# Performance work log

Measured on AMD Instinct MI355X. Metric: run time of the kernel, lower is better.

The kernel has to match this reference:

```python
import jax, jax.numpy as jnp
import numpy as np

HEADS = 16
HIDDEN = 1024
DH = HIDDEN // HEADS
EPS = 1e-6


def setup_inputs() -> dict:
    key = jax.random.key(0)
    ks = jax.random.split(key, 18)
    B, S, D, H = 8, 4096, HIDDEN, HEADS
    std = 0.02
    inp = {
        "x": jax.random.normal(ks[0], (B, S, D), dtype=jnp.float32),
        "mask": jnp.zeros((B, 1, S), dtype=jnp.float32),
        "Wq": std * jax.random.normal(ks[1], (D, D), dtype=jnp.float32),
        "bq": jnp.zeros((D,), jnp.float32),
        "Wk": std * jax.random.normal(ks[2], (D, D), dtype=jnp.float32),
        "bk": jnp.zeros((D,), jnp.float32),
        "Wv": std * jax.random.normal(ks[3], (D, D), dtype=jnp.float32),
        "bv": jnp.zeros((D,), jnp.float32),
        "Wa": std * jax.random.normal(ks[4], (D, H), dtype=jnp.float32),
        "ba": jnp.zeros((H,), jnp.float32),
        "Wb": std * jax.random.normal(ks[5], (D, H), dtype=jnp.float32),
        "bb": jnp.zeros((H,), jnp.float32),
        "Wu": std * jax.random.normal(ks[6], (D, D), dtype=jnp.float32),
        "bu": jnp.zeros((D,), jnp.float32),
        "Wo": std * jax.random.normal(ks[7], (D, D), dtype=jnp.float32),
        "bo": jnp.zeros((D,), jnp.float32),
        "ln_g": jnp.ones((D,), jnp.float32),
        "ln_b": jnp.zeros((D,), jnp.float32),
    }
    return inp


def reference(x, mask, Wq, bq, Wk, bk, Wv, bv, Wa, ba, Wb, bb, Wu, bu, Wo, bo, ln_g, ln_b):
    B, S, D = x.shape
    H, dh = HEADS, D // HEADS
    scale = (D / H) ** -0.5

    q = x @ Wq + bq  # [B,S,D]
    k = x @ Wk + bk
    v = x @ Wv + bv

    # alpha pooling of q
    ascore = jnp.swapaxes((q @ Wa + ba) * scale, 1, 2) + mask  # [B,H,S]
    aw = jax.nn.softmax(ascore, axis=-1)
    qh = q.reshape(B, S, H, dh)
    q_av = jnp.einsum("bhs,bshd->bhd", aw, qh).reshape(B, 1, D)  # global query

    p = k * q_av  # [B,S,D], broadcast over seq

    # beta pooling of p
    bscore = jnp.swapaxes((p @ Wb + bb) * scale, 1, 2) + mask  # [B,H,S]
    bw = jax.nn.softmax(bscore, axis=-1)
    ph = p.reshape(B, S, H, dh)
    p_av = jnp.einsum("bhs,bshd->bhd", bw, ph).reshape(B, 1, D)  # global key

    u = p_av * v  # [B,S,D]
    r = u @ Wu + bu
    attn_out = (r + q) @ Wo + bo

    y = x + attn_out  # residual (dropout is identity at inference)
    mu = jnp.mean(y, axis=-1, keepdims=True)
    var = jnp.mean(jnp.square(y - mu), axis=-1, keepdims=True)
    return (y - mu) * jax.lax.rsqrt(var + EPS) * ln_g + ln_b
```

## Files before the change

### kernel.cpp

```cpp
#include <hip/hip_runtime.h>

typedef unsigned short u16;
typedef __bf16 bf16x8 __attribute__((ext_vector_type(8)));
typedef float  f32x4  __attribute__((ext_vector_type(4)));

__device__ __forceinline__ float b2f(u16 u) {
    unsigned int v = ((unsigned int)u) << 16;
    return __builtin_bit_cast(float, v);
}
__device__ __forceinline__ u16 f2b(float f) {
    unsigned int v = __builtin_bit_cast(unsigned int, f);
    v += 0x7fffu + ((v >> 16) & 1u);
    return (u16)(v >> 16);
}

#define GLD16(gp, lp) __builtin_amdgcn_global_load_lds( \
    (const __attribute__((address_space(1))) void*)(gp), \
    (__attribute__((address_space(3))) void*)(lp), 16, 0, 0)


__global__ __launch_bounds__(256) void convert_x(const float* __restrict__ x,
                                                 u16* __restrict__ xb) {
    size_t i = ((size_t)blockIdx.x * 256 + threadIdx.x) * 8;
    float4 v0 = *(const float4*)(x + i);
    float4 v1 = *(const float4*)(x + i + 4);
    ushort4 o0, o1;
    o0.x = f2b(v0.x); o0.y = f2b(v0.y); o0.z = f2b(v0.z); o0.w = f2b(v0.w);
    o1.x = f2b(v1.x); o1.y = f2b(v1.y); o1.z = f2b(v1.z); o1.w = f2b(v1.w);
    *(ushort4*)(xb + i)     = o0;
    *(ushort4*)(xb + i + 4) = o1;
}

__global__ __launch_bounds__(256) void transpose_w(const float* __restrict__ W,
                                                   u16* __restrict__ Wt) {
    __shared__ float tile[64][65];
    int kt = (blockIdx.x & 15) * 64;
    int nt = (blockIdx.x >> 4) * 64;
    int tid = threadIdx.x;
    int r = tid >> 4, c4 = (tid & 15) * 4;
    #pragma unroll
    for (int p = 0; p < 4; ++p) {
        int k = kt + p * 16 + r;
        float4 v = *(const float4*)(W + (size_t)k * 1024 + nt + c4);
        tile[c4 + 0][p * 16 + r] = v.x;
        tile[c4 + 1][p * 16 + r] = v.y;
        tile[c4 + 2][p * 16 + r] = v.z;
        tile[c4 + 3][p * 16 + r] = v.w;
    }
    __syncthreads();
    #pragma unroll
    for (int p = 0; p < 4; ++p) {
        int nl = p * 16 + r;
        ushort4 o;
        o.x = f2b(tile[nl][c4 + 0]); o.y = f2b(tile[nl][c4 + 1]);
        o.z = f2b(tile[nl][c4 + 2]); o.w = f2b(tile[nl][c4 + 3]);
        *(ushort4*)(Wt + (size_t)(nt + nl) * 1024 + kt + c4) = o;
    }
}

__global__ __launch_bounds__(256) void wu_prime(const float* __restrict__ Wu,
                                                const float* __restrict__ p_av,
                                                u16* __restrict__ Wut) {
    __shared__ float tile[64][65];
    int kt = (blockIdx.x & 15) * 64;
    int nt = (blockIdx.x >> 4) * 64;
    int tid = threadIdx.x;
    int r = tid >> 4, c4 = (tid & 15) * 4;
    #pragma unroll
    for (int p = 0; p < 4; ++p) {
        int k = kt + p * 16 + r;
        float4 v = *(const float4*)(Wu + (size_t)k * 1024 + nt + c4);
        tile[c4 + 0][p * 16 + r] = v.x;
        tile[c4 + 1][p * 16 + r] = v.y;
        tile[c4 + 2][p * 16 + r] = v.z;
        tile[c4 + 3][p * 16 + r] = v.w;
    }
    __syncthreads();
    for (int b = 0; b < 8; ++b) {
        float4 pv = *(const float4*)(p_av + (size_t)b * 1024 + kt + c4);
        #pragma unroll
        for (int p = 0; p < 4; ++p) {
            int nl = p * 16 + r;
            ushort4 o;
            o.x = f2b(tile[nl][c4 + 0] * pv.x);
            o.y = f2b(tile[nl][c4 + 1] * pv.y);
            o.z = f2b(tile[nl][c4 + 2] * pv.z);
            o.w = f2b(tile[nl][c4 + 3] * pv.w);
            *(ushort4*)(Wut + ((size_t)b * 1024 + nt + nl) * 1024 + kt + c4) = o;
        }
    }
}

__global__ __launch_bounds__(256) void wat_prep(const float* __restrict__ Wa,
                                                u16* __restrict__ Wat) {
    int idx = blockIdx.x * 256 + threadIdx.x;
    int h = idx >> 10, k = idx & 1023;
    Wat[idx] = f2b(Wa[(k << 4) + h]);
}

__global__ __launch_bounds__(256) void wbt_prep(const float* __restrict__ Wb,
                                                const float* __restrict__ q_av,
                                                u16* __restrict__ Wbt) {
    int idx = blockIdx.x * 256 + threadIdx.x;
    int b = idx >> 14, rem = idx & 16383;
    int h = rem >> 10, k = rem & 1023;
    Wbt[idx] = f2b(Wb[(k << 4) + h] * q_av[(b << 10) + k]);
}

__global__ __launch_bounds__(256) void bias_concat(const float* __restrict__ bq,
                                                   const float* __restrict__ bk,
                                                   const float* __restrict__ bv,
                                                   float* __restrict__ outb) {
    int i = blockIdx.x * 256 + threadIdx.x;
    outb[i] = (i < 1024) ? bq[i] : (i < 2048 ? bk[i - 1024] : bv[i - 2048]);
}

__global__ __launch_bounds__(256, 4)
void gemm_bf16(const u16* __restrict__ A, int lda,
               const u16* __restrict__ Bt,
               const float* __restrict__ bias,
               const u16* __restrict__ addsrc, int ldadd,
               u16* __restrict__ C, int ldc,
               int N, int K, int batch_rows) {
    __shared__ u16 As[128 * 64];
    __shared__ u16 Bs[128 * 64];
    int ntiles = N >> 7;
    int bid = blockIdx.x;
    int mtiles = gridDim.x / ntiles;
    int tm, tn;
    if ((mtiles & 7) == 0) {
        int xcd = bid & 7, s = bid >> 3;
        int mper = mtiles >> 3;
        tm = xcd * mper + s / ntiles;
        tn = s - (s / ntiles) * ntiles;
    } else {
        tm = bid / ntiles; tn = bid - (bid / ntiles) * ntiles;
    }
    int m0 = tm << 7, n0 = tn << 7;
    if (batch_rows > 0) Bt += (size_t)(m0 / batch_rows) * (size_t)N * K;
    int tid = threadIdx.x, lane = tid & 63, w = tid >> 6;
    int wm = (w >> 1) << 6, wn = (w & 1) << 6;
    int quad = lane >> 4, l16 = lane & 15;
    int rph = l16 & 7;
    int lrow = lane >> 3;
    int lkg  = (lane & 7) ^ lrow;

    int idxA = (m0 + (w << 5) + lrow) * lda + (lkg << 3);
    int idxB = (n0 + (w << 5) + lrow) * K   + (lkg << 3);
    int stepA = lda << 3, stepB = K << 3;

    f32x4 zero = {0.f, 0.f, 0.f, 0.f};
    f32x4 acc[4][4];
    #pragma unroll
    for (int i = 0; i < 4; ++i)
        #pragma unroll
        for (int j = 0; j < 4; ++j) acc[i][j] = zero;

    for (int kt = 0; kt < K; kt += 64) {
        __syncthreads();
        #pragma unroll
        for (int j = 0; j < 4; ++j) {
            int c = (w << 2) + j;
            GLD16(A  + (idxA + j * stepA + kt), &As[c << 9]);
            GLD16(Bt + (idxB + j * stepB + kt), &Bs[c << 9]);
        }
        __syncthreads();
        #pragma unroll
        for (int kk = 0; kk < 2; ++kk) {
            bf16x8 a[4], b[4];
            int kg = (((kk << 2) + quad) ^ rph) << 3;
            #pragma unroll
            for (int i = 0; i < 4; ++i) {
                a[i] = *(const bf16x8*)&As[((wm + (i << 4) + l16) << 6) + kg];
                b[i] = *(const bf16x8*)&Bs[((wn + (i << 4) + l16) << 6) + kg];
            }
            #pragma unroll
            for (int mi = 0; mi < 4; ++mi)
                #pragma unroll
                for (int ni = 0; ni < 4; ++ni)
                    acc[mi][ni] = __builtin_amdgcn_mfma_f32_16x16x32_bf16(
                        a[mi], b[ni], acc[mi][ni], 0, 0, 0);
        }
    }
    #pragma unroll
    for (int mi = 0; mi < 4; ++mi) {
        #pragma unroll
        for (int ni = 0; ni < 4; ++ni) {
            int col = n0 + wn + (ni << 4) + l16;
            float bv = bias[col];
            #pragma unroll
            for (int rg = 0; rg < 4; ++rg) {
                int rowg = m0 + wm + (mi << 4) + (quad << 2) + rg;
                float vv = acc[mi][ni][rg] + bv;
                if (addsrc) vv += b2f(addsrc[(size_t)rowg * ldadd + col]);
                C[(size_t)rowg * ldc + col] = f2b(vv);
            }
        }
    }
}

__global__ __launch_bounds__(256)
void score_gemm(const u16* __restrict__ A, int lda,
                const u16* __restrict__ Bt,
                const float* __restrict__ bias16,
                const float* __restrict__ mask,
                float* __restrict__ outsc,
                int batched) {
    __shared__ u16 As[64 * 64];
    __shared__ u16 Bs[16 * 64];
    int m0 = blockIdx.x << 6;
    int tid = threadIdx.x, lane = tid & 63, w = tid >> 6;
    int quad = lane >> 4, l16 = lane & 15;
    int rph = l16 & 7;
    int lrow = lane >> 3;
    int lkg  = (lane & 7) ^ lrow;
    const u16* Bb = Bt + (batched ? ((size_t)(m0 >> 12) << 14) : 0);

    int idxA = (m0 + (w << 4) + lrow) * lda + (lkg << 3);
    int stepA = lda << 3;
    int idxB = lrow * 1024 + (lkg << 3);

    f32x4 acc4 = (f32x4){0.f, 0.f, 0.f, 0.f};

    for (int kt = 0; kt < 1024; kt += 64) {
        __syncthreads();
        #pragma unroll
        for (int j = 0; j < 2; ++j) {
            int c = (w << 1) + j;
            GLD16(A + (idxA + j * stepA + kt), &As[c << 9]);
        }
        if (w < 2)
            GLD16(Bb + (idxB + w * 8192 + kt), &Bs[w << 9]);
        __syncthreads();
        #pragma unroll
        for (int kk = 0; kk < 2; ++kk) {
            int kg = (((kk << 2) + quad) ^ rph) << 3;
            bf16x8 b = *(const bf16x8*)&Bs[(l16 << 6) + kg];
            bf16x8 a = *(const bf16x8*)&As[(((w << 4) + l16) << 6) + kg];
            acc4 = __builtin_amdgcn_mfma_f32_16x16x32_bf16(a, b, acc4, 0, 0, 0);
        }
    }
    int bidx = m0 >> 12;
    float bv = bias16[l16];
    float* orow = outsc + (((size_t)bidx << 4) + l16) * 4096;
    const float* mrow = mask + ((size_t)bidx << 12);
    int sbase = (m0 & 4095) + (w << 4) + (quad << 2);
    #pragma unroll
    for (int rg = 0; rg < 4; ++rg)
        orow[sbase + rg] = 0.125f * (acc4[rg] + bv) + mrow[sbase + rg];
}

__global__ __launch_bounds__(256)
void softmax_kernel(float* __restrict__ score) {
    __shared__ float wbuf[4096];
    __shared__ float red[4];
    int tid = threadIdx.x, lane = tid & 63, w = tid >> 6;
    float* srow = score + (size_t)blockIdx.x * 4096;
    float mx = -1e30f;
    for (int s = tid; s < 4096; s += 256) mx = fmaxf(mx, srow[s]);
    for (int o = 32; o; o >>= 1) mx = fmaxf(mx, __shfl_xor(mx, o));
    if (lane == 0) red[w] = mx;
    __syncthreads();
    mx = fmaxf(fmaxf(red[0], red[1]), fmaxf(red[2], red[3]));
    __syncthreads();
    float sm = 0.f;
    for (int s = tid; s < 4096; s += 256) {
        float e = __expf(srow[s] - mx);
        wbuf[s] = e;
        sm += e;
    }
    for (int o = 32; o; o >>= 1) sm += __shfl_xor(sm, o);
    if (lane == 0) red[w] = sm;
    __syncthreads();
    float inv = 1.f / (red[0] + red[1] + red[2] + red[3]);
    for (int s = tid; s < 4096; s += 256) srow[s] = wbuf[s] * inv;
}

__global__ __launch_bounds__(256)
void pool_sum(const float* __restrict__ wn,
              const u16* __restrict__ X, int ldx,
              float* __restrict__ part) {
    __shared__ float psum[16][64];
    int blk = blockIdx.x, tid = threadIdx.x;
    int cc = blk & 7, bh = blk >> 3;
    int b = bh >> 4, h = bh & 15;
    const float* wrow = wn + ((size_t)bh << 12) + (cc << 9);
    int dg = (tid & 15) << 2;
    int sc = tid >> 4;
    const u16* base = X + (size_t)((b << 12) + (cc << 9) + (sc << 5)) * ldx + (h << 6) + dg;
    float a0 = 0, a1 = 0, a2 = 0, a3 = 0;
    for (int s = 0; s < 32; ++s) {
        float wv = wrow[(sc << 5) + s];
        ushort4 uv = *(const ushort4*)(base + (size_t)s * ldx);
        a0 += wv * b2f(uv.x); a1 += wv * b2f(uv.y);
        a2 += wv * b2f(uv.z); a3 += wv * b2f(uv.w);
    }
    psum[sc][dg + 0] = a0; psum[sc][dg + 1] = a1;
    psum[sc][dg + 2] = a2; psum[sc][dg + 3] = a3;
    __syncthreads();
    if (tid < 64) {
        float t = 0.f;
        #pragma unroll
        for (int j = 0; j < 16; ++j) t += psum[j][tid];
        part[(((size_t)bh << 3) + cc) * 64 + tid] = t;
    }
}

__global__ __launch_bounds__(256)
void pool_finalize(const float* __restrict__ part,
                   const float* __restrict__ mul,
                   float* __restrict__ outav) {
    int idx = blockIdx.x * 256 + threadIdx.x;
    const float* p = part + ((size_t)(idx >> 6) << 9) + (idx & 63);
    float s = 0.f;
    #pragma unroll
    for (int c = 0; c < 8; ++c) s += p[c << 6];
    if (mul) s *= mul[idx];
    outav[idx] = s;
}

__global__ __launch_bounds__(256)
void ln_kernel(const u16* __restrict__ Z, const float* __restrict__ g,
               const float* __restrict__ bta, float* __restrict__ outp) {
    __shared__ float rs1[4], rs2[4];
    int row = blockIdx.x, tid = threadIdx.x;
    const u16* zr = Z + ((size_t)row << 10);
    ushort4 uv = *(const ushort4*)(zr + (tid << 2));
    float v0 = b2f(uv.x), v1 = b2f(uv.y), v2 = b2f(uv.z), v3 = b2f(uv.w);
    float s = v0 + v1 + v2 + v3;
    float s2 = v0 * v0 + v1 * v1 + v2 * v2 + v3 * v3;
    for (int o = 32; o; o >>= 1) { s += __shfl_xor(s, o); s2 += __shfl_xor(s2, o); }
    if ((tid & 63) == 0) { rs1[tid >> 6] = s; rs2[tid >> 6] = s2; }
    __syncthreads();
    float S = rs1[0] + rs1[1] + rs1[2] + rs1[3];
    float S2 = rs2[0] + rs2[1] + rs2[2] + rs2[3];
    float mean = S * (1.0f / 1024.0f);
    float var = S2 * (1.0f / 1024.0f) - mean * mean;
    float inv = rsqrtf(var + 1e-6f);
    int c = tid << 2;
    float4 o4;
    o4.x = (v0 - mean) * inv * g[c + 0] + bta[c + 0];
    o4.y = (v1 - mean) * inv * g[c + 1] + bta[c + 1];
    o4.z = (v2 - mean) * inv * g[c + 2] + bta[c + 2];
    o4.w = (v3 - mean) * inv * g[c + 3] + bta[c + 3];
    *(float4*)(outp + ((size_t)row << 10) + c) = o4;
}


extern "C" void kernel_launch(void* const* d_in, const int* in_sizes, int n_in,
                              void* d_out, int out_size, void* d_ws, size_t ws_size,
                              hipStream_t stream) {
    (void)in_sizes; (void)n_in; (void)out_size;
    const float* x    = (const float*)d_in[0];
    const float* mask = (const float*)d_in[1];
    const float* Wq   = (const float*)d_in[2];
    const float* bq   = (const float*)d_in[3];
    const float* Wk   = (const float*)d_in[4];
    const float* bk   = (const float*)d_in[5];
    const float* Wv   = (const float*)d_in[6];
    const float* bv   = (const float*)d_in[7];
    const float* Wa   = (const float*)d_in[8];
    const float* ba   = (const float*)d_in[9];
    const float* Wb   = (const float*)d_in[10];
    const float* bb   = (const float*)d_in[11];
    const float* Wu   = (const float*)d_in[12];
    const float* bu   = (const float*)d_in[13];
    const float* Wo   = (const float*)d_in[14];
    const float* bo   = (const float*)d_in[15];
    const float* ln_g = (const float*)d_in[16];
    const float* ln_b = (const float*)d_in[17];
    float* outp = (float*)d_out;

    char* ws = (char*)d_ws;
    u16*   xb    = (u16*)(ws);
    u16*   qkv   = (u16*)(ws + 67108864);
    u16*   Wqkvt = (u16*)(ws + 268435456);
    u16*   Wot   = (u16*)(ws + 274726912);
    u16*   Wat   = (u16*)(ws + 276824064);
    u16*   Wbt   = (u16*)(ws + 276856832);
    float* score = (float*)(ws + 277118976);
    float* q_av  = (float*)(ws + 279216128);
    float* p_av  = (float*)(ws + 279248896);
    float* biasq = (float*)(ws + 279281664);
    u16*   Wubt  = (u16*)(ws + 279293952);
    float* part  = (float*)(ws + 296071168);
    if (ws_size < 296333312ULL) return;

    convert_x<<<16384, 256, 0, stream>>>(x, xb);
    transpose_w<<<256, 256, 0, stream>>>(Wq, Wqkvt);
    transpose_w<<<256, 256, 0, stream>>>(Wk, Wqkvt + 1048576);
    transpose_w<<<256, 256, 0, stream>>>(Wv, Wqkvt + 2097152);
    transpose_w<<<256, 256, 0, stream>>>(Wo, Wot);
    wat_prep<<<64, 256, 0, stream>>>(Wa, Wat);
    bias_concat<<<12, 256, 0, stream>>>(bq, bk, bv, biasq);

    gemm_bf16<<<6144, 256, 0, stream>>>(xb, 1024, Wqkvt, biasq,
                                        nullptr, 0, qkv, 3072, 3072, 1024, 0);
    score_gemm<<<512, 256, 0, stream>>>(qkv, 3072, Wat, ba, mask, score, 0);
    softmax_kernel<<<128, 256, 0, stream>>>(score);
    pool_sum<<<1024, 256, 0, stream>>>(score, qkv, 3072, part);
    pool_finalize<<<32, 256, 0, stream>>>(part, nullptr, q_av);
    wbt_prep<<<512, 256, 0, stream>>>(Wb, q_av, Wbt);
    score_gemm<<<512, 256, 0, stream>>>(qkv + 1024, 3072, Wbt, bb, mask, score, 1);
    softmax_kernel<<<128, 256, 0, stream>>>(score);
    pool_sum<<<1024, 256, 0, stream>>>(score, qkv + 1024, 3072, part);
    pool_finalize<<<32, 256, 0, stream>>>(part, q_av, p_av);
    wu_prime<<<256, 256, 0, stream>>>(Wu, p_av, Wubt);
    gemm_bf16<<<2048, 256, 0, stream>>>(qkv + 2048, 3072, Wubt, bu,
                                        qkv, 3072, qkv, 3072, 1024, 1024, 4096);
    gemm_bf16<<<2048, 256, 0, stream>>>(qkv, 3072, Wot, bo,
                                        xb, 1024, xb, 1024, 1024, 1024, 0);
    ln_kernel<<<32768, 256, 0, stream>>>(xb, ln_g, ln_b, outp);
}
```

Baseline: 850.3 us.

## Fuse softmax into score GEMM and pooling; merge weight prep kernels

Drops the standalone softmax kernel. The score GEMM now writes per-block partial row maxima, and pool_sum folds the global max, the exponentials and the partial exp sums into its weighted accumulation. pool_finalize divides by the summed denominators. The four weight transposes, the Wa prep and the bias concat are also merged into one launch. This removes two full passes over the score buffer and several small launches, at the cost of an extra cross-block max reduction and more work inside the pooling kernel.

```diff
diff --git a/kernel.cpp b/kernel.cpp
--- a/kernel.cpp
+++ b/kernel.cpp
@@ -31,30 +31,49 @@
     *(ushort4*)(xb + i + 4) = o1;
 }
 
-__global__ __launch_bounds__(256) void transpose_w(const float* __restrict__ W,
-                                                   u16* __restrict__ Wt) {
+__global__ __launch_bounds__(256)
+void prep_all(const float* __restrict__ Wq, const float* __restrict__ Wk,
+              const float* __restrict__ Wv, const float* __restrict__ Wo,
+              u16* __restrict__ Wqkvt, u16* __restrict__ Wot,
+              const float* __restrict__ Wa, u16* __restrict__ Wat,
+              const float* __restrict__ bq, const float* __restrict__ bk,
+              const float* __restrict__ bv, float* __restrict__ biasq) {
     __shared__ float tile[64][65];
-    int kt = (blockIdx.x & 15) * 64;
-    int nt = (blockIdx.x >> 4) * 64;
+    int blk = blockIdx.x;
     int tid = threadIdx.x;
-    int r = tid >> 4, c4 = (tid & 15) * 4;
-    #pragma unroll
-    for (int p = 0; p < 4; ++p) {
-        int k = kt + p * 16 + r;
-        float4 v = *(const float4*)(W + (size_t)k * 1024 + nt + c4);
-        tile[c4 + 0][p * 16 + r] = v.x;
-        tile[c4 + 1][p * 16 + r] = v.y;
-        tile[c4 + 2][p * 16 + r] = v.z;
-        tile[c4 + 3][p * 16 + r] = v.w;
-    }
-    __syncthreads();
-    #pragma unroll
-    for (int p = 0; p < 4; ++p) {
-        int nl = p * 16 + r;
-        ushort4 o;
-        o.x = f2b(tile[nl][c4 + 0]); o.y = f2b(tile[nl][c4 + 1]);
-        o.z = f2b(tile[nl][c4 + 2]); o.w = f2b(tile[nl][c4 + 3]);
-        *(ushort4*)(Wt + (size_t)(nt + nl) * 1024 + kt + c4) = o;
+    if (blk < 1024) {
+        int g = blk >> 8;
+        int lb = blk & 255;
+        const float* W = (g == 0) ? Wq : (g == 1) ? Wk : (g == 2) ? Wv : Wo;
+        u16* Wt = (g == 3) ? Wot : (Wqkvt + (size_t)g * 1048576);
+        int kt = (lb & 15) * 64;
+        int nt = (lb >> 4) * 64;
+        int r = tid >> 4, c4 = (tid & 15) * 4;
+        #pragma unroll
+        for (int p = 0; p < 4; ++p) {
+            int k = kt + p * 16 + r;
+            float4 v = *(const float4*)(W + (size_t)k * 1024 + nt + c4);
+            tile[c4 + 0][p * 16 + r] = v.x;
+            tile[c4 + 1][p * 16 + r] = v.y;
+            tile[c4 + 2][p * 16 + r] = v.z;
+            tile[c4 + 3][p * 16 + r] = v.w;
+        }
+        __syncthreads();
+        #pragma unroll
+        for (int p = 0; p < 4; ++p) {
+            int nl = p * 16 + r;
+            ushort4 o;
+            o.x = f2b(tile[nl][c4 + 0]); o.y = f2b(tile[nl][c4 + 1]);
+            o.z = f2b(tile[nl][c4 + 2]); o.w = f2b(tile[nl][c4 + 3]);
+            *(ushort4*)(Wt + (size_t)(nt + nl) * 1024 + kt + c4) = o;
+        }
+    } else if (blk < 1088) {
+        int idx = (blk - 1024) * 256 + tid;
+        int h = idx >> 10, k = idx & 1023;
+        Wat[idx] = f2b(Wa[(k << 4) + h]);
+    } else {
+        int i = (blk - 1088) * 256 + tid;
+        biasq[i] = (i < 1024) ? bq[i] : (i < 2048 ? bk[i - 1024] : bv[i - 2048]);
     }
 }
 
@@ -91,13 +110,6 @@
     }
 }
 
-__global__ __launch_bounds__(256) void wat_prep(const float* __restrict__ Wa,
-                                                u16* __restrict__ Wat) {
-    int idx = blockIdx.x * 256 + threadIdx.x;
-    int h = idx >> 10, k = idx & 1023;
-    Wat[idx] = f2b(Wa[(k << 4) + h]);
-}
-
 __global__ __launch_bounds__(256) void wbt_prep(const float* __restrict__ Wb,
                                                 const float* __restrict__ q_av,
                                                 u16* __restrict__ Wbt) {
@@ -105,14 +117,6 @@
     int b = idx >> 14, rem = idx & 16383;
     int h = rem >> 10, k = rem & 1023;
     Wbt[idx] = f2b(Wb[(k << 4) + h] * q_av[(b << 10) + k]);
-}
-
-__global__ __launch_bounds__(256) void bias_concat(const float* __restrict__ bq,
-                                                   const float* __restrict__ bk,
-                                                   const float* __restrict__ bv,
-                                                   float* __restrict__ outb) {
-    int i = blockIdx.x * 256 + threadIdx.x;
-    outb[i] = (i < 1024) ? bq[i] : (i < 2048 ? bk[i - 1024] : bv[i - 2048]);
 }
 
 __global__ __launch_bounds__(256, 4)
@@ -205,9 +209,11 @@
                 const float* __restrict__ bias16,
                 const float* __restrict__ mask,
                 float* __restrict__ outsc,
+                float* __restrict__ pmax,
                 int batched) {
     __shared__ u16 As[64 * 64];
     __shared__ u16 Bs[16 * 64];
+    __shared__ float pm[16][16];
     int m0 = blockIdx.x << 6;
     int tid = threadIdx.x, lane = tid & 63, w = tid >> 6;
     int quad = lane >> 4, l16 = lane & 15;
@@ -245,58 +251,57 @@
     float* orow = outsc + (((size_t)bidx << 4) + l16) * 4096;
     const float* mrow = mask + ((size_t)bidx << 12);
     int sbase = (m0 & 4095) + (w << 4) + (quad << 2);
+    float lm = -1e30f;
     #pragma unroll
-    for (int rg = 0; rg < 4; ++rg)
-        orow[sbase + rg] = 0.125f * (acc4[rg] + bv) + mrow[sbase + rg];
+    for (int rg = 0; rg < 4; ++rg) {
+        float sv = 0.125f * (acc4[rg] + bv) + mrow[sbase + rg];
+        orow[sbase + rg] = sv;
+        lm = fmaxf(lm, sv);
+    }
+    pm[(w << 2) | quad][l16] = lm;
+    __syncthreads();
+    if (tid < 16) {
+        float m = pm[0][tid];
+        #pragma unroll
+        for (int j = 1; j < 16; ++j) m = fmaxf(m, pm[j][tid]);
+        pmax[(((bidx << 4) + tid) << 6) + (blockIdx.x & 63)] = m;
+    }
 }
 
 __global__ __launch_bounds__(256)
-void softmax_kernel(float* __restrict__ score) {
-    __shared__ float wbuf[4096];
-    __shared__ float red[4];
-    int tid = threadIdx.x, lane = tid & 63, w = tid >> 6;
-    float* srow = score + (size_t)blockIdx.x * 4096;
-    float mx = -1e30f;
-    for (int s = tid; s < 4096; s += 256) mx = fmaxf(mx, srow[s]);
-    for (int o = 32; o; o >>= 1) mx = fmaxf(mx, __shfl_xor(mx, o));
-    if (lane == 0) red[w] = mx;
-    __syncthreads();
-    mx = fmaxf(fmaxf(red[0], red[1]), fmaxf(red[2], red[3]));
-    __syncthreads();
-    float sm = 0.f;
-    for (int s = tid; s < 4096; s += 256) {
-        float e = __expf(srow[s] - mx);
-        wbuf[s] = e;
-        sm += e;
-    }
-    for (int o = 32; o; o >>= 1) sm += __shfl_xor(sm, o);
-    if (lane == 0) red[w] = sm;
-    __syncthreads();
-    float inv = 1.f / (red[0] + red[1] + red[2] + red[3]);
-    for (int s = tid; s < 4096; s += 256) srow[s] = wbuf[s] * inv;
-}
-
-__global__ __launch_bounds__(256)
-void pool_sum(const float* __restrict__ wn,
+void pool_sum(const float* __restrict__ score,
+              const float* __restrict__ pmax,
               const u16* __restrict__ X, int ldx,
-              float* __restrict__ part) {
+              float* __restrict__ part,
+              float* __restrict__ parte) {
     __shared__ float psum[16][64];
+    __shared__ float pes[16];
+    __shared__ float smx;
     int blk = blockIdx.x, tid = threadIdx.x;
     int cc = blk & 7, bh = blk >> 3;
     int b = bh >> 4, h = bh & 15;
-    const float* wrow = wn + ((size_t)bh << 12) + (cc << 9);
+    if (tid < 64) {
+        float m = pmax[(bh << 6) + tid];
+        for (int o = 32; o; o >>= 1) m = fmaxf(m, __shfl_xor(m, o));
+        if (tid == 0) smx = m;
+    }
+    __syncthreads();
+    float mx = smx;
+    const float* wrow = score + ((size_t)bh << 12) + (cc << 9);
     int dg = (tid & 15) << 2;
     int sc = tid >> 4;
     const u16* base = X + (size_t)((b << 12) + (cc << 9) + (sc << 5)) * ldx + (h << 6) + dg;
-    float a0 = 0, a1 = 0, a2 = 0, a3 = 0;
+    float a0 = 0, a1 = 0, a2 = 0, a3 = 0, es = 0;
     for (int s = 0; s < 32; ++s) {
-        float wv = wrow[(sc << 5) + s];
+        float e = __expf(wrow[(sc << 5) + s] - mx);
+        es += e;
         ushort4 uv = *(const ushort4*)(base + (size_t)s * ldx);
-        a0 += wv * b2f(uv.x); a1 += wv * b2f(uv.y);
-        a2 += wv * b2f(uv.z); a3 += wv * b2f(uv.w);
+        a0 += e * b2f(uv.x); a1 += e * b2f(uv.y);
+        a2 += e * b2f(uv.z); a3 += e * b2f(uv.w);
     }
     psum[sc][dg + 0] = a0; psum[sc][dg + 1] = a1;
     psum[sc][dg + 2] = a2; psum[sc][dg + 3] = a3;
+    if ((tid & 15) == 0) pes[sc] = es;
     __syncthreads();
     if (tid < 64) {
         float t = 0.f;
@@ -304,17 +309,27 @@
         for (int j = 0; j < 16; ++j) t += psum[j][tid];
         part[(((size_t)bh << 3) + cc) * 64 + tid] = t;
     }
+    if (tid == 64) {
+        float e = 0.f;
+        #pragma unroll
+        for (int j = 0; j < 16; ++j) e += pes[j];
+        parte[(bh << 3) + cc] = e;
+    }
 }
 
 __global__ __launch_bounds__(256)
 void pool_finalize(const float* __restrict__ part,
+                   const float* __restrict__ parte,
                    const float* __restrict__ mul,
                    float* __restrict__ outav) {
     int idx = blockIdx.x * 256 + threadIdx.x;
-    const float* p = part + ((size_t)(idx >> 6) << 9) + (idx & 63);
-    float s = 0.f;
+    int bh = idx >> 6;
+    const float* p = part + ((size_t)bh << 9) + (idx & 63);
+    const float* pe = parte + (bh << 3);
+    float s = 0.f, e = 0.f;
     #pragma unroll
-    for (int c = 0; c < 8; ++c) s += p[c << 6];
+    for (int c = 0; c < 8; ++c) { s += p[c << 6]; e += pe[c]; }
+    s /= e;
     if (mul) s *= mul[idx];
     outav[idx] = s;
 }
@@ -384,27 +399,23 @@
     float* biasq = (float*)(ws + 279281664);
     u16*   Wubt  = (u16*)(ws + 279293952);
     float* part  = (float*)(ws + 296071168);
-    if (ws_size < 296333312ULL) return;
+    float* pmax  = (float*)(ws + 296333312);
+    float* parte = (float*)(ws + 296366080);
+    if (ws_size < 296370176ULL) return;
 
     convert_x<<<16384, 256, 0, stream>>>(x, xb);
-    transpose_w<<<256, 256, 0, stream>>>(Wq, Wqkvt);
-    transpose_w<<<256, 256, 0, stream>>>(Wk, Wqkvt + 1048576);
-    transpose_w<<<256, 256, 0, stream>>>(Wv, Wqkvt + 2097152);
-    transpose_w<<<256, 256, 0, stream>>>(Wo, Wot);
-    wat_prep<<<64, 256, 0, stream>>>(Wa, Wat);
-    bias_concat<<<12, 256, 0, stream>>>(bq, bk, bv, biasq);
+    prep_all<<<1100, 256, 0, stream>>>(Wq, Wk, Wv, Wo, Wqkvt, Wot, Wa, Wat,
+                                       bq, bk, bv, biasq);
 
     gemm_bf16<<<6144, 256, 0, stream>>>(xb, 1024, Wqkvt, biasq,
                                         nullptr, 0, qkv, 3072, 3072, 1024, 0);
-    score_gemm<<<512, 256, 0, stream>>>(qkv, 3072, Wat, ba, mask, score, 0);
-    softmax_kernel<<<128, 256, 0, stream>>>(score);
-    pool_sum<<<1024, 256, 0, stream>>>(score, qkv, 3072, part);
-    pool_finalize<<<32, 256, 0, stream>>>(part, nullptr, q_av);
+    score_gemm<<<512, 256, 0, stream>>>(qkv, 3072, Wat, ba, mask, score, pmax, 0);
+    pool_sum<<<1024, 256, 0, stream>>>(score, pmax, qkv, 3072, part, parte);
+    pool_finalize<<<32, 256, 0, stream>>>(part, parte, nullptr, q_av);
     wbt_prep<<<512, 256, 0, stream>>>(Wb, q_av, Wbt);
-    score_gemm<<<512, 256, 0, stream>>>(qkv + 1024, 3072, Wbt, bb, mask, score, 1);
-    softmax_kernel<<<128, 256, 0, stream>>>(score);
-    pool_sum<<<1024, 256, 0, stream>>>(score, qkv + 1024, 3072, part);
-    pool_finalize<<<32, 256, 0, stream>>>(part, q_av, p_av);
+    score_gemm<<<512, 256, 0, stream>>>(qkv + 1024, 3072, Wbt, bb, mask, score, pmax, 1);
+    pool_sum<<<1024, 256, 0, stream>>>(score, pmax, qkv + 1024, 3072, part, parte);
+    pool_finalize<<<32, 256, 0, stream>>>(part, parte, q_av, p_av);
     wu_prime<<<256, 256, 0, stream>>>(Wu, p_av, Wubt);
     gemm_bf16<<<2048, 256, 0, stream>>>(qkv + 2048, 3072, Wubt, bu,
                                         qkv, 3072, qkv, 3072, 1024, 1024, 4096);
```

Result: no change. 836.0 us (-1.7%).
